# Performance work log

Measured on AMD Instinct MI355X. Metric: run time of the kernel, lower is better.

## Reference

```python
import jax, jax.numpy as jnp
import numpy as np

ALPHA = 0.5
NUM_NB = 8


def setup_inputs() -> dict:
    key = jax.random.key(0)
    k1, k2 = jax.random.split(key)
    pc1 = jax.random.normal(k1, (4, 3, 8192), dtype=jnp.float32)
    pred_flow = jax.random.normal(k2, (4, 3, 8192), dtype=jnp.float32)
    return {"pc1": pc1, "pred_flow": pred_flow}


def reference(pc1, pred_flow):
    # pc1, pred_flow: [B, 3, N] -> [B, N, 3]
    B, _, N = pc1.shape
    k = NUM_NB
    p = jnp.transpose(pc1, (0, 2, 1))         # [B, N, 3]
    f = jnp.transpose(pred_flow, (0, 2, 1))   # [B, N, 3]

    sq = jnp.sum(p * p, axis=-1)
    sqrdist = sq[:, :, None] + sq[:, None, :] - 2.0 * jnp.einsum('bnd,bmd->bnm', p, p)

    # k+1 smallest (sorted ascending), drop self (first column)
    neg_d, kidx = jax.lax.top_k(-sqrdist, k + 1)  # descending in -d == ascending in d
    dists = -neg_d[:, :, 1:]                      # [B, N, k]
    kidx = kidx[:, :, 1:]                         # [B, N, k]
    dists = jnp.maximum(dists, 0.0)

    # softmax over all N*k weights per batch
    w = jax.nn.softmax(jnp.exp(-dists / ALPHA).reshape(B, N * k), axis=1)
    w = w.reshape(B, N, k)

    # gather neighbor flows: [B, N, k, 3]
    grouped = jnp.take_along_axis(f[:, None, :, :],
                                  kidx[:, :, :, None],
                                  axis=2)
    diff = jnp.linalg.norm(grouped - f[:, :, None, :], axis=3)  # [B, N, k]
    diff_flow = (N * w * diff).sum(axis=2)                      # [B, N]
    return jnp.mean(diff_flow)
```

## Files before the change

### kernel.cpp

```cpp
#include <hip/hip_runtime.h>
#include <hip/hip_bf16.h>
#include <math.h>

#define BATCH 4
#define NQ 8192
#define KNB 8
#define K1 9
#define CAP 34
#define THSAMP 256
#define SPART 2
#define IDXMASK 8191u
#define KEYMASK 0xFFFFE000u
#define EPS_S 1e-3f

#define CHAIN9(KEY) { unsigned kk = (KEY); \
  _Pragma("unroll") \
  for (int j = 0; j < K1; ++j) { \
    unsigned lo = min(kk, nk[j]); unsigned hi = max(kk, nk[j]); \
    nk[j] = lo; kk = hi; } }

#define DRAIN() { \
  for (int i = 0; i < cnt; ++i) { \
    int j = sbuf[base + i]; \
    float dx = qx - px[j], dy = qy - py[j], dz = qz - pz[j]; \
    float d = dx*dx + dy*dy + dz*dz; \
    unsigned key = (__float_as_uint(d) & KEYMASK) | (unsigned)j; \
    if (key < nk[K1-1]) CHAIN9(key); \
  } \
  cnt = 0; \
  if (nk[K1-1] != 0xFFFFFFFFu) { \
    float td = __uint_as_float(nk[K1-1] | 0x1FFFu); \
    thetaS = fminf(thetaS, 0.5f*(td - qq) + EPS_S); \
  } }

#define GPROC(SS, GIDX) { \
  if ((SS) <= thetaS) { sbuf[base + cnt] = (unsigned short)(GIDX); cnt++; } }

#define SCORE4(S0,S1,S2,S3, X,Y,Z,H) \
  float S0 = fmaf(nqx, X.x, fmaf(nqy, Y.x, fmaf(nqz, Z.x, H.x))); \
  float S1 = fmaf(nqx, X.y, fmaf(nqy, Y.y, fmaf(nqz, Z.y, H.y))); \
  float S2 = fmaf(nqx, X.z, fmaf(nqy, Y.z, fmaf(nqz, Z.z, H.z))); \
  float S3 = fmaf(nqx, X.w, fmaf(nqy, Y.w, fmaf(nqz, Z.w, H.w)));

__global__ __launch_bounds__(256) void theta_kernel(
    const float* __restrict__ pc, unsigned* __restrict__ thetaOut,
    float* __restrict__ hOut)
{
  __shared__ float swx[THSAMP], swy[THSAMP], swz[THSAMP];
  const int b = blockIdx.y, p = blockIdx.z;
  const int q = blockIdx.x * 256 + threadIdx.x;
  const float* __restrict__ px = pc + (size_t)b * 3 * NQ;
  const float* __restrict__ py = px + NQ;
  const float* __restrict__ pz = px + 2 * NQ;
  const int tid = threadIdx.x;
  const int si = tid * (NQ / THSAMP) + p * (NQ / THSAMP / SPART);
  swx[tid] = px[si]; swy[tid] = py[si]; swz[tid] = pz[si];
  __syncthreads();
  const float qx = px[q], qy = py[q], qz = pz[q];
  if (p == 0) hOut[b * NQ + q] = 0.5f * (qx*qx + qy*qy + qz*qz);
  unsigned nk[K1];
#pragma unroll
  for (int j = 0; j < K1; ++j) nk[j] = 0xFFFFFFFFu;
  for (int i = 0; i < THSAMP; ++i) {
    float dx = qx - swx[i], dy = qy - swy[i], dz = qz - swz[i];
    float d = dx * dx + dy * dy + dz * dz;
    CHAIN9(__float_as_uint(d));
  }
  thetaOut[(size_t)(b * NQ + q) * SPART + p] = nk[K1 - 1] | 0x1FFFu;
}

__global__ __launch_bounds__(256) void knn_kernel(
    const float* __restrict__ pc, const float* __restrict__ hB,
    const unsigned* __restrict__ thetaIn, unsigned* __restrict__ wsK,
    int P, int cpp)
{
  __shared__ unsigned short sbuf[256 * CAP];
  const int b = blockIdx.y;
  const int p = blockIdx.z;
  const int q = blockIdx.x * 256 + threadIdx.x;
  const float* __restrict__ px = pc + (size_t)b * 3 * NQ;
  const float* __restrict__ py = px + NQ;
  const float* __restrict__ pz = px + 2 * NQ;
  const float* __restrict__ ph = hB + (size_t)b * NQ;
  const float4* __restrict__ px4 = (const float4*)px;
  const float4* __restrict__ py4 = (const float4*)py;
  const float4* __restrict__ pz4 = (const float4*)pz;
  const float4* __restrict__ ph4 = (const float4*)ph;
  const float qx = px[q], qy = py[q], qz = pz[q];
  const float nqx = -qx, nqy = -qy, nqz = -qz;
  const float qq = qx*qx + qy*qy + qz*qz;

  uint2 th = ((const uint2*)thetaIn)[b * NQ + q];
  float thetaS = 0.5f * (__uint_as_float(min(th.x, th.y)) - qq) + EPS_S;

  unsigned nk[K1];
#pragma unroll
  for (int j = 0; j < K1; ++j) nk[j] = 0xFFFFFFFFu;

  const unsigned base = (unsigned)threadIdx.x * CAP;
  int cnt = 0;
  const int c0 = p * cpp;

  for (int t = 0; t < cpp; t += 8) {
    if (__any(cnt >= CAP - 8)) { DRAIN(); }
    const int ti = (c0 + t) >> 2;
    const float4 X0 = px4[ti], X1 = px4[ti + 1];
    const float4 Y0 = py4[ti], Y1 = py4[ti + 1];
    const float4 Z0 = pz4[ti], Z1 = pz4[ti + 1];
    const float4 H0 = ph4[ti], H1 = ph4[ti + 1];
    SCORE4(s0, s1, s2, s3, X0, Y0, Z0, H0);
    SCORE4(s4, s5, s6, s7, X1, Y1, Z1, H1);
    const int g = c0 + t;
    GPROC(s0, g + 0); GPROC(s1, g + 1); GPROC(s2, g + 2); GPROC(s3, g + 3);
    GPROC(s4, g + 4); GPROC(s5, g + 5); GPROC(s6, g + 6); GPROC(s7, g + 7);
  }
  DRAIN();

#pragma unroll
  for (int j = 0; j < K1; ++j)
    wsK[((size_t)(b * P + p) * K1 + j) * NQ + q] = nk[j];
}

__global__ __launch_bounds__(256) void loss_kernel(
    const float* __restrict__ pc, const float* __restrict__ pf,
    const unsigned* __restrict__ wsK, float* __restrict__ acc, int P)
{
  const int b = blockIdx.y;
  const int q = blockIdx.x * 256 + threadIdx.x;
  const float* __restrict__ px = pc + (size_t)b * 3 * NQ;
  const float* __restrict__ py = px + NQ;
  const float* __restrict__ pz = px + 2 * NQ;
  const float* __restrict__ fx = pf + (size_t)b * 3 * NQ;
  const float* __restrict__ fy = fx + NQ;
  const float* __restrict__ fz = fx + 2 * NQ;

  unsigned nk[KNB];
#pragma unroll
  for (int j = 0; j < KNB; ++j) nk[j] = 0xFFFFFFFFu;

  const int total = P * K1;
  for (int m = 0; m < total; ++m) {
    unsigned key = wsK[((size_t)b * P * K1 + m) * NQ + q];
    if ((key & IDXMASK) == (unsigned)q) continue;
    if (key < nk[KNB - 1]) {
      unsigned kk = key;
#pragma unroll
      for (int j = 0; j < KNB; ++j) {
        unsigned lo = min(kk, nk[j]); unsigned hi = max(kk, nk[j]);
        nk[j] = lo; kk = hi;
      }
    }
  }

  const float qx = px[q], qy = py[q], qz = pz[q];
  const float fqx = fx[q], fqy = fy[q], fqz = fz[q];
  float ssum = 0.f, sdsum = 0.f;
#pragma unroll
  for (int j = 0; j < KNB; ++j) {
    int i = (int)(nk[j] & IDXMASK);
    float dx = qx - px[i], dy = qy - py[i], dz = qz - pz[i];
    float d = dx * dx + dy * dy + dz * dz;
    float e = expf(expf(-2.0f * d));
    float gx = fx[i] - fqx, gy = fy[i] - fqy, gz = fz[i] - fqz;
    float diff = sqrtf(gx * gx + gy * gy + gz * gz);
    ssum += e; sdsum += e * diff;
  }

  for (int off = 32; off > 0; off >>= 1) {
    ssum += __shfl_down(ssum, off);
    sdsum += __shfl_down(sdsum, off);
  }
  __shared__ float r[8];
  const int lane = threadIdx.x & 63, wid = threadIdx.x >> 6;
  if (lane == 0) { r[wid * 2] = ssum; r[wid * 2 + 1] = sdsum; }
  __syncthreads();
  if (threadIdx.x == 0) {
    float s0 = r[0] + r[2] + r[4] + r[6];
    float s1 = r[1] + r[3] + r[5] + r[7];
    atomicAdd(&acc[b * 2 + 0], s0);
    atomicAdd(&acc[b * 2 + 1], s1);
  }
}

__global__ void final_kernel(const float* __restrict__ acc, float* __restrict__ out)
{
  if (threadIdx.x == 0) {
    float s = 0.f;
    for (int b = 0; b < BATCH; ++b) s += acc[b * 2 + 1] / acc[b * 2];
    out[0] = s * (1.0f / BATCH);
  }
}

extern "C" void kernel_launch(void* const* d_in, const int* in_sizes, int n_in,
                              void* d_out, int out_size, void* d_ws, size_t ws_size,
                              hipStream_t stream) {
  const float* pc = (const float*)d_in[0];
  const float* pf = (const float*)d_in[1];
  float* out = (float*)d_out;
  float* acc = (float*)d_ws;
  const size_t thetaBytes = (size_t)BATCH * NQ * SPART * sizeof(unsigned);
  const size_t hBytes = (size_t)BATCH * NQ * sizeof(float);
  unsigned* thetaBuf = (unsigned*)((char*)d_ws + 256);
  float* hBuf = (float*)((char*)d_ws + 256 + thetaBytes);
  unsigned* wsK = (unsigned*)((char*)d_ws + 256 + thetaBytes + hBytes);

  const size_t fixed = 256 + thetaBytes + hBytes;
  const size_t needP16 = fixed + (size_t)BATCH * NQ * 16 * K1 * sizeof(unsigned);
  const size_t needP8  = fixed + (size_t)BATCH * NQ * 8  * K1 * sizeof(unsigned);
  const size_t needP4  = fixed + (size_t)BATCH * NQ * 4  * K1 * sizeof(unsigned);
  const int P = (ws_size >= needP16) ? 16 : (ws_size >= needP8) ? 8
              : (ws_size >= needP4) ? 4 : 1;
  const int cpp = NQ / P;

  hipMemsetAsync(d_ws, 0, 256, stream);

  dim3 g0(NQ / 256, BATCH, SPART);
  theta_kernel<<<g0, 256, 0, stream>>>(pc, thetaBuf, hBuf);

  dim3 g1(NQ / 256, BATCH, P);
  knn_kernel<<<g1, 256, 0, stream>>>(pc, hBuf, thetaBuf, wsK, P, cpp);

  dim3 g2(NQ / 256, BATCH);
  loss_kernel<<<g2, 256, 0, stream>>>(pc, pf, wsK, acc, P);

  final_kernel<<<1, 64, 0, stream>>>(acc, out);
}
```

Baseline: 148.1 us.

## Widen knn scan unroll, batch loss key loads, fuse final reduction into loss

The knn candidate scan now handles 16 points per iteration instead of 8, giving the compiler more independent loads and work per drain check. The loss kernel loads nine keys at once before merging them, runs at 64 threads per block so the shared-memory reduction and syncthreads go away, and ends with a last-block-done counter so the final division runs inside it instead of in a separate final kernel. This saves one kernel launch and some load latency. The cost is higher register pressure and more candidates appended per step before a drain, which triggers more frequent drains given CAP of 34.

```diff
diff --git a/kernel.cpp b/kernel.cpp
--- a/kernel.cpp
+++ b/kernel.cpp
@@ -16,6 +16,12 @@
 #define CHAIN9(KEY) { unsigned kk = (KEY); \
   _Pragma("unroll") \
   for (int j = 0; j < K1; ++j) { \
+    unsigned lo = min(kk, nk[j]); unsigned hi = max(kk, nk[j]); \
+    nk[j] = lo; kk = hi; } }
+
+#define CHAIN8(KEY) { unsigned kk = (KEY); \
+  _Pragma("unroll") \
+  for (int j = 0; j < KNB; ++j) { \
     unsigned lo = min(kk, nk[j]); unsigned hi = max(kk, nk[j]); \
     nk[j] = lo; kk = hi; } }
 
@@ -101,18 +107,22 @@
   int cnt = 0;
   const int c0 = p * cpp;
 
-  for (int t = 0; t < cpp; t += 8) {
-    if (__any(cnt >= CAP - 8)) { DRAIN(); }
+  for (int t = 0; t < cpp; t += 16) {
+    if (__any(cnt >= CAP - 16)) { DRAIN(); }
     const int ti = (c0 + t) >> 2;
-    const float4 X0 = px4[ti], X1 = px4[ti + 1];
-    const float4 Y0 = py4[ti], Y1 = py4[ti + 1];
-    const float4 Z0 = pz4[ti], Z1 = pz4[ti + 1];
-    const float4 H0 = ph4[ti], H1 = ph4[ti + 1];
+    const float4 X0 = px4[ti],     X1 = px4[ti + 1], X2 = px4[ti + 2], X3 = px4[ti + 3];
+    const float4 Y0 = py4[ti],     Y1 = py4[ti + 1], Y2 = py4[ti + 2], Y3 = py4[ti + 3];
+    const float4 Z0 = pz4[ti],     Z1 = pz4[ti + 1], Z2 = pz4[ti + 2], Z3 = pz4[ti + 3];
+    const float4 H0 = ph4[ti],     H1 = ph4[ti + 1], H2 = ph4[ti + 2], H3 = ph4[ti + 3];
     SCORE4(s0, s1, s2, s3, X0, Y0, Z0, H0);
     SCORE4(s4, s5, s6, s7, X1, Y1, Z1, H1);
+    SCORE4(s8, s9, sa, sb, X2, Y2, Z2, H2);
+    SCORE4(sc, sd, se, sf, X3, Y3, Z3, H3);
     const int g = c0 + t;
-    GPROC(s0, g + 0); GPROC(s1, g + 1); GPROC(s2, g + 2); GPROC(s3, g + 3);
-    GPROC(s4, g + 4); GPROC(s5, g + 5); GPROC(s6, g + 6); GPROC(s7, g + 7);
+    GPROC(s0, g + 0);  GPROC(s1, g + 1);  GPROC(s2, g + 2);  GPROC(s3, g + 3);
+    GPROC(s4, g + 4);  GPROC(s5, g + 5);  GPROC(s6, g + 6);  GPROC(s7, g + 7);
+    GPROC(s8, g + 8);  GPROC(s9, g + 9);  GPROC(sa, g + 10); GPROC(sb, g + 11);
+    GPROC(sc, g + 12); GPROC(sd, g + 13); GPROC(se, g + 14); GPROC(sf, g + 15);
   }
   DRAIN();
 
@@ -121,12 +131,14 @@
     wsK[((size_t)(b * P + p) * K1 + j) * NQ + q] = nk[j];
 }
 
-__global__ __launch_bounds__(256) void loss_kernel(
+__global__ __launch_bounds__(64) void loss_kernel(
     const float* __restrict__ pc, const float* __restrict__ pf,
-    const unsigned* __restrict__ wsK, float* __restrict__ acc, int P)
+    const unsigned* __restrict__ wsK, float* __restrict__ acc,
+    unsigned* __restrict__ doneCtr, float* __restrict__ out,
+    int P, int nBlocks)
 {
   const int b = blockIdx.y;
-  const int q = blockIdx.x * 256 + threadIdx.x;
+  const int q = blockIdx.x * 64 + threadIdx.x;
   const float* __restrict__ px = pc + (size_t)b * 3 * NQ;
   const float* __restrict__ py = px + NQ;
   const float* __restrict__ pz = px + 2 * NQ;
@@ -139,16 +151,17 @@
   for (int j = 0; j < KNB; ++j) nk[j] = 0xFFFFFFFFu;
 
   const int total = P * K1;
-  for (int m = 0; m < total; ++m) {
-    unsigned key = wsK[((size_t)b * P * K1 + m) * NQ + q];
-    if ((key & IDXMASK) == (unsigned)q) continue;
-    if (key < nk[KNB - 1]) {
-      unsigned kk = key;
-#pragma unroll
-      for (int j = 0; j < KNB; ++j) {
-        unsigned lo = min(kk, nk[j]); unsigned hi = max(kk, nk[j]);
-        nk[j] = lo; kk = hi;
-      }
+  const size_t stride0 = (size_t)b * P * K1;
+  for (int m0 = 0; m0 < total; m0 += K1) {
+    unsigned kb[K1];
+#pragma unroll
+    for (int u = 0; u < K1; ++u)
+      kb[u] = wsK[(stride0 + m0 + u) * NQ + q];
+#pragma unroll
+    for (int u = 0; u < K1; ++u) {
+      unsigned key = kb[u];
+      if ((key & IDXMASK) == (unsigned)q) continue;
+      if (key < nk[KNB - 1]) CHAIN8(key);
     }
   }
 
@@ -170,24 +183,20 @@
     ssum += __shfl_down(ssum, off);
     sdsum += __shfl_down(sdsum, off);
   }
-  __shared__ float r[8];
-  const int lane = threadIdx.x & 63, wid = threadIdx.x >> 6;
-  if (lane == 0) { r[wid * 2] = ssum; r[wid * 2 + 1] = sdsum; }
-  __syncthreads();
   if (threadIdx.x == 0) {
-    float s0 = r[0] + r[2] + r[4] + r[6];
-    float s1 = r[1] + r[3] + r[5] + r[7];
-    atomicAdd(&acc[b * 2 + 0], s0);
-    atomicAdd(&acc[b * 2 + 1], s1);
-  }
-}
-
-__global__ void final_kernel(const float* __restrict__ acc, float* __restrict__ out)
-{
-  if (threadIdx.x == 0) {
-    float s = 0.f;
-    for (int b = 0; b < BATCH; ++b) s += acc[b * 2 + 1] / acc[b * 2];
-    out[0] = s * (1.0f / BATCH);
+    atomicAdd(&acc[b * 2 + 0], ssum);
+    atomicAdd(&acc[b * 2 + 1], sdsum);
+    __threadfence();
+    unsigned done = atomicAdd(doneCtr, 1u);
+    if (done == (unsigned)(nBlocks - 1)) {
+      float s = 0.f;
+      for (int bb = 0; bb < BATCH; ++bb) {
+        float se = atomicAdd(&acc[bb * 2 + 0], 0.f);
+        float sd = atomicAdd(&acc[bb * 2 + 1], 0.f);
+        s += sd / se;
+      }
+      out[0] = s * (1.0f / BATCH);
+    }
   }
 }
 
@@ -198,6 +207,7 @@
   const float* pf = (const float*)d_in[1];
   float* out = (float*)d_out;
   float* acc = (float*)d_ws;
+  unsigned* doneCtr = (unsigned*)((char*)d_ws + 64);
   const size_t thetaBytes = (size_t)BATCH * NQ * SPART * sizeof(unsigned);
   const size_t hBytes = (size_t)BATCH * NQ * sizeof(float);
   unsigned* thetaBuf = (unsigned*)((char*)d_ws + 256);
@@ -220,8 +230,7 @@
   dim3 g1(NQ / 256, BATCH, P);
   knn_kernel<<<g1, 256, 0, stream>>>(pc, hBuf, thetaBuf, wsK, P, cpp);
 
-  dim3 g2(NQ / 256, BATCH);
-  loss_kernel<<<g2, 256, 0, stream>>>(pc, pf, wsK, acc, P);
-
-  final_kernel<<<1, 64, 0, stream>>>(acc, out);
-}
+  dim3 g2(NQ / 64, BATCH);
+  const int nBlocks = (NQ / 64) * BATCH;
+  loss_kernel<<<g2, 64, 0, stream>>>(pc, pf, wsK, acc, doneCtr, out, P, nBlocks);
+}
```

Result: faster. 142.8 us (-3.6%).
